# Performance work log

Hardware: AMD Instinct MI355X
Metric: run time of the kernel (lower is better)

The kernel has to match this reference:

```python
import jax, jax.numpy as jnp
import numpy as np


def gru_cell(x, h, Wi, Wh, bi, bh):
    # PyTorch GRU gate order: r, z, n
    gi = x @ Wi + bi
    gh = h @ Wh + bh
    ir, iz, inn = jnp.split(gi, 3, axis=-1)
    hr, hz, hn = jnp.split(gh, 3, axis=-1)
    r = jax.nn.sigmoid(ir + hr)
    z = jax.nn.sigmoid(iz + hz)
    n = jnp.tanh(inn + r * hn)
    return (1.0 - z) * n + z * h


def run_gru_dir(emb, lens, Wi, Wh, bi, bh, reverse):
    # Masked GRU emulating pack_padded_sequence: state holds once t >= len,
    # padded output positions are zero (as pad_packed_sequence produces).
    B, S, _ = emb.shape
    H = Wh.shape[0]
    xs = jnp.swapaxes(emb, 0, 1)  # [S, B, E]
    ts = jnp.arange(S)
    if reverse:
        xs = xs[::-1]
        ts = ts[::-1]
    def step(h, inp):
        x, t = inp
        valid = (t < lens)[:, None]
        h_new = jnp.where(valid, gru_cell(x, h, Wi, Wh, bi, bh), h)
        return h_new, jnp.where(valid, h_new, 0.0)
    hT, outs = jax.lax.scan(step, jnp.zeros((B, H), emb.dtype), (xs, ts))
    if reverse:
        outs = outs[::-1]
    return jnp.swapaxes(outs, 0, 1), hT  # [B,S,H], [B,H]


def seq2seq_forward(src, trg, src_lens, enc_embed, Wi_f, Wh_f, bi_f, bh_f,
                    Wi_b, Wh_b, bi_b, bh_b, W_e2d, b_e2d, dec_embed,
                    Wi_d, Wh_d, bi_d, bh_d, Wq, bq, Wk, bk, Wv, bv,
                    W1, b1, W2, b2):
    lens = jnp.clip(src_lens, 1, None)
    emb = enc_embed[src]  # [B,S,E]; dropout is identity in eval
    out_f, h_f = run_gru_dir(emb, lens, Wi_f, Wh_f, bi_f, bh_f, False)
    out_b, h_b = run_gru_dir(emb, lens, Wi_b, Wh_b, bi_b, bh_b, True)
    word_reps = jnp.concatenate([out_f, out_b], axis=-1)  # [B,S,2H]
    sent_rep = jnp.concatenate([h_f, h_b], axis=-1)       # [B,2H]
    hidden0 = jax.nn.gelu(sent_rep @ W_e2d + b_e2d, approximate=False)
    # k/v projections are loop-invariant -> hoist (same math as per-step)
    K = word_reps @ Wk + bk   # [B,S,kq]
    V = word_reps @ Wv + bv   # [B,S,D]
    scale = 1.0 / np.sqrt(Wq.shape[1]).astype(np.float32)
    def dec_step(h_prev, tok):
        e = dec_embed[tok]  # [B,E]
        h = gru_cell(e, h_prev, Wi_d, Wh_d, bi_d, bh_d)
        q = h @ Wq + bq
        alpha = jax.nn.softmax(jnp.einsum('bk,bsk->bs', q, K) * scale, axis=-1)
        attn = jnp.einsum('bs,bsd->bd', alpha, V)
        hid = h + attn
        out = jax.nn.gelu(hid @ W1 + b1, approximate=False) @ W2 + b2
        return hid, out
    toks = trg[:, :-1].T  # [T-1, B]
    _, outs = jax.lax.scan(dec_step, hidden0, toks)  # [T-1, B, V]
    B = trg.shape[0]
    V = W2.shape[1]
    # outputs[:, 0, :] stays zero as in the original preallocated buffer
    return jnp.concatenate(
        [jnp.zeros((B, 1, V), outs.dtype), jnp.swapaxes(outs, 0, 1)], axis=1)


def setup_inputs() -> dict:
    key = jax.random.key(0)
    ks = iter(jax.random.split(key, 32))
    B, S, T = 32, 64, 64
    SV, TV, E, H, D, KQ = 32000, 32000, 256, 512, 512, 64
    def nrm(shape, fan_in):
        return jax.random.normal(next(ks), shape, jnp.float32) / np.sqrt(fan_in).astype(np.float32)
    return {
        'src': jax.random.randint(next(ks), (B, S), 0, SV),
        'trg': jax.random.randint(next(ks), (B, T), 0, TV),
        'src_lens': jax.random.randint(next(ks), (B,), 1, S + 1),
        'enc_embed': jax.random.normal(next(ks), (SV, E), jnp.float32) * 0.1,
        'Wi_f': nrm((E, 3 * H), E), 'Wh_f': nrm((H, 3 * H), H),
        'bi_f': jnp.zeros((3 * H,), jnp.float32), 'bh_f': jnp.zeros((3 * H,), jnp.float32),
        'Wi_b': nrm((E, 3 * H), E), 'Wh_b': nrm((H, 3 * H), H),
        'bi_b': jnp.zeros((3 * H,), jnp.float32), 'bh_b': jnp.zeros((3 * H,), jnp.float32),
        'W_e2d': nrm((2 * H, D), 2 * H), 'b_e2d': jnp.zeros((D,), jnp.float32),
        'dec_embed': jax.random.normal(next(ks), (TV, E), jnp.float32) * 0.1,
        'Wi_d': nrm((E, 3 * D), E), 'Wh_d': nrm((D, 3 * D), D),
        'bi_d': jnp.zeros((3 * D,), jnp.float32), 'bh_d': jnp.zeros((3 * D,), jnp.float32),
        'Wq': nrm((D, KQ), D), 'bq': jnp.zeros((KQ,), jnp.float32),
        'Wk': nrm((2 * H, KQ), 2 * H), 'bk': jnp.zeros((KQ,), jnp.float32),
        'Wv': nrm((2 * H, D), 2 * H), 'bv': jnp.zeros((D,), jnp.float32),
        'W1': nrm((D, D), D), 'b1': jnp.zeros((D,), jnp.float32),
        'W2': nrm((D, TV), D), 'b2': jnp.zeros((TV,), jnp.float32),
    }


def reference(src, trg, src_lens, enc_embed, Wi_f, Wh_f, bi_f, bh_f,
              Wi_b, Wh_b, bi_b, bh_b, W_e2d, b_e2d, dec_embed,
              Wi_d, Wh_d, bi_d, bh_d, Wq, bq, Wk, bk, Wv, bv,
              W1, b1, W2, b2):
    return seq2seq_forward(src, trg, src_lens, enc_embed, Wi_f, Wh_f, bi_f, bh_f,
                           Wi_b, Wh_b, bi_b, bh_b, W_e2d, b_e2d, dec_embed,
                           Wi_d, Wh_d, bi_d, bh_d, Wq, bq, Wk, bk, Wv, bv,
                           W1, b1, W2, b2)
```

## Files before the change

### kernel.cpp

```cpp
#include <hip/hip_runtime.h>
#include <stdint.h>

typedef unsigned short u16;
typedef short v8s __attribute__((ext_vector_type(8)));
typedef float v4f __attribute__((ext_vector_type(4)));

#define DI static __device__ __forceinline__

DI u16 f2bf(float x){ union{float f; uint32_t u;} c; c.f = x; uint32_t r = c.u + 0x7fffu + ((c.u >> 16) & 1u); return (u16)(r >> 16); }
DI float bf2f(u16 b){ union{float f; uint32_t u;} c; c.u = ((uint32_t)b) << 16; return c.f; }
DI float gelu_f(float x){ return 0.5f * x * (1.0f + erff(x * 0.70710678118654752f)); }
DI float sigm(float x){ return 1.0f / (1.0f + expf(-x)); }

__global__ __launch_bounds__(256) void transpose_split_kernel(
    const float* __restrict__ W, u16* __restrict__ hi, u16* __restrict__ lo, int K, int N)
{
    __shared__ float t[32][33];
    int n0 = blockIdx.x * 32, k0 = blockIdx.y * 32;
    int tx = threadIdx.x & 31, ty = threadIdx.x >> 5;
    #pragma unroll
    for (int i = 0; i < 4; i++) {
        int k = k0 + ty + i * 8, n = n0 + tx;
        float v = (k < K && n < N) ? W[(size_t)k * N + n] : 0.f;
        t[ty + i * 8][tx] = v;
    }
    __syncthreads();
    #pragma unroll
    for (int i = 0; i < 4; i++) {
        int n = n0 + ty + i * 8, k = k0 + tx;
        if (n < N && k < K) {
            float v = t[tx][ty + i * 8];
            u16 h = f2bf(v);
            hi[(size_t)n * K + k] = h;
            lo[(size_t)n * K + k] = f2bf(v - bf2f(h));
        }
    }
}

__global__ __launch_bounds__(256) void gather_init_kernel(
    const int* __restrict__ src, const int* __restrict__ trg,
    const float* __restrict__ enc_embed, const float* __restrict__ dec_embed,
    float* __restrict__ embE, float* __restrict__ embD,
    float* __restrict__ hF0, float* __restrict__ hB0)
{
    int r = blockIdx.x, tx = threadIdx.x;
    if (r < 2048) {
        int idx = src[r];
        embE[(size_t)r * 256 + tx] = enc_embed[(size_t)idx * 256 + tx];
    } else if (r < 4064) {
        int rd = r - 2048;
        int t = rd >> 5, b = rd & 31;
        int tok = trg[b * 64 + t];
        embD[(size_t)rd * 256 + tx] = dec_embed[(size_t)tok * 256 + tx];
    } else {
        int i = (r - 4064) * 256 + tx;
        if (i < 16384) hF0[i] = 0.f; else hB0[i - 16384] = 0.f;
    }
}

__global__ __launch_bounds__(256) void gemm_bf16x3_kernel(
    const float* __restrict__ A, const u16* __restrict__ Bhi, const u16* __restrict__ Blo,
    const float* __restrict__ bias, float* __restrict__ C,
    int M, int N, int K, int act_gelu, int remap)
{
    __shared__ u16 Ah[128 * 40], Al[128 * 40], Bh[128 * 40], Bl[128 * 40];
    const int tid = threadIdx.x;
    const int lane = tid & 63, wave = tid >> 6;
    const int lm = lane & 15, quad = lane >> 4;
    const int wm = wave >> 1, wn = wave & 1;
    const int m0 = blockIdx.y * 128, n0 = blockIdx.x * 128;
    const int sr = tid >> 1;
    const int sh = (tid & 1) * 16;

    v4f acc[4][4];
    #pragma unroll
    for (int i = 0; i < 4; i++)
        #pragma unroll
        for (int j = 0; j < 4; j++)
            #pragma unroll
            for (int r = 0; r < 4; r++) acc[i][j][r] = 0.f;

    for (int k0 = 0; k0 < K; k0 += 32) {
        {
            float v[16];
            const int gm = m0 + sr;
            if (gm < M) {
                const float4* p = (const float4*)(A + (size_t)gm * K + k0 + sh);
                #pragma unroll
                for (int i = 0; i < 4; i++) {
                    float4 q = p[i];
                    v[4*i] = q.x; v[4*i+1] = q.y; v[4*i+2] = q.z; v[4*i+3] = q.w;
                }
            } else {
                #pragma unroll
                for (int i = 0; i < 16; i++) v[i] = 0.f;
            }
            v8s h0, h1, l0, l1;
            #pragma unroll
            for (int i = 0; i < 8; i++) {
                u16 ha = f2bf(v[i]);     u16 la = f2bf(v[i] - bf2f(ha));
                u16 hb = f2bf(v[8+i]);   u16 lb = f2bf(v[8+i] - bf2f(hb));
                h0[i] = (short)ha; l0[i] = (short)la; h1[i] = (short)hb; l1[i] = (short)lb;
            }
            *(v8s*)&Ah[sr * 40 + sh] = h0; *(v8s*)&Ah[sr * 40 + sh + 8] = h1;
            *(v8s*)&Al[sr * 40 + sh] = l0; *(v8s*)&Al[sr * 40 + sh + 8] = l1;
        }
        {
            const int gn = n0 + sr;
            v8s b0, b1, c0, c1;
            if (gn < N) {
                const v8s* ph = (const v8s*)(Bhi + (size_t)gn * K + k0 + sh);
                const v8s* pl = (const v8s*)(Blo + (size_t)gn * K + k0 + sh);
                b0 = ph[0]; b1 = ph[1]; c0 = pl[0]; c1 = pl[1];
            } else {
                #pragma unroll
                for (int i = 0; i < 8; i++) { b0[i] = 0; b1[i] = 0; c0[i] = 0; c1[i] = 0; }
            }
            *(v8s*)&Bh[sr * 40 + sh] = b0; *(v8s*)&Bh[sr * 40 + sh + 8] = b1;
            *(v8s*)&Bl[sr * 40 + sh] = c0; *(v8s*)&Bl[sr * 40 + sh + 8] = c1;
        }
        __syncthreads();
        v8s ah[4], al[4], bh[4], bl[4];
        #pragma unroll
        for (int mt = 0; mt < 4; mt++) {
            int off = (wm * 64 + mt * 16 + lm) * 40 + quad * 8;
            ah[mt] = *(v8s*)&Ah[off]; al[mt] = *(v8s*)&Al[off];
        }
        #pragma unroll
        for (int nt = 0; nt < 4; nt++) {
            int off = (wn * 64 + nt * 16 + lm) * 40 + quad * 8;
            bh[nt] = *(v8s*)&Bh[off]; bl[nt] = *(v8s*)&Bl[off];
        }
        #pragma unroll
        for (int mt = 0; mt < 4; mt++)
            #pragma unroll
            for (int nt = 0; nt < 4; nt++) {
                v4f a = acc[mt][nt];
                a = __builtin_amdgcn_mfma_f32_16x16x32_bf16(ah[mt], bh[nt], a, 0, 0, 0);
                a = __builtin_amdgcn_mfma_f32_16x16x32_bf16(ah[mt], bl[nt], a, 0, 0, 0);
                a = __builtin_amdgcn_mfma_f32_16x16x32_bf16(al[mt], bh[nt], a, 0, 0, 0);
                acc[mt][nt] = a;
            }
        __syncthreads();
    }
    #pragma unroll
    for (int nt = 0; nt < 4; nt++) {
        int col = n0 + wn * 64 + nt * 16 + lm;
        if (col >= N) continue;
        float bv = bias ? bias[col] : 0.f;
        #pragma unroll
        for (int mt = 0; mt < 4; mt++) {
            int rbase = m0 + wm * 64 + mt * 16 + quad * 4;
            #pragma unroll
            for (int r = 0; r < 4; r++) {
                int row = rbase + r;
                if (row < M) {
                    float v = acc[mt][nt][r] + bv;
                    if (act_gelu) v = gelu_f(v);
                    size_t drow = remap ? (size_t)((row & 31) * 64 + (row >> 5) + 1) : (size_t)row;
                    C[drow * (size_t)N + col] = v;
                }
            }
        }
    }
}

DI float gru_out(float i0, float i1, float i2, float g0, float g1, float g2,
                 float b0, float b1, float b2, float hprev)
{
    float r = sigm(i0 + g0 + b0);
    float z = sigm(i1 + g1 + b1);
    float n = tanhf(i2 + r * (g2 + b2));
    return (1.f - z) * n + z * hprev;
}

__global__ __launch_bounds__(256) void enc_step_kernel(
    int step,
    const float* __restrict__ hFin, float* __restrict__ hFout,
    const float* __restrict__ hBin, float* __restrict__ hBout,
    const float* __restrict__ giF, const float* __restrict__ giB,
    const float* __restrict__ Wh_f, const float* __restrict__ Wh_b,
    const float* __restrict__ bh_f, const float* __restrict__ bh_b,
    const int* __restrict__ src_lens,
    float* __restrict__ wrep, float* __restrict__ sent)
{
    const int dir = blockIdx.x >> 6;
    const int jb = (blockIdx.x & 63) * 8;
    const int tid = threadIdx.x;
    const int b = tid >> 3, jj = tid & 7, j = jb + jj;
    const float* hin = dir ? hBin : hFin;
    const float* gi  = dir ? giB : giF;
    const float* Wh  = dir ? Wh_b : Wh_f;
    const float* bh  = dir ? bh_b : bh_f;
    float* hout = dir ? hBout : hFout;
    const int t_eff = dir ? (63 - step) : step;

    __shared__ float hl[32 * 132];
    float g0 = 0.f, g1 = 0.f, g2 = 0.f;
    for (int kt = 0; kt < 512; kt += 128) {
        __syncthreads();
        #pragma unroll
        for (int w = 0; w < 4; w++) {
            int flat = (tid + w * 256) * 4;
            int bb = flat >> 7, kk = flat & 127;
            float4 fv = *(const float4*)(hin + bb * 512 + kt + kk);
            *(float4*)&hl[bb * 132 + kk] = fv;
        }
        __syncthreads();
        const float* w0base = Wh + (size_t)kt * 1536 + j;
        #pragma unroll 2
        for (int kk = 0; kk < 128; kk += 4) {
            float4 hv = *(const float4*)&hl[b * 132 + kk];
            const float* w = w0base + (size_t)kk * 1536;
            g0 += hv.x * w[0];    g1 += hv.x * w[512];  g2 += hv.x * w[1024];
            g0 += hv.y * w[1536]; g1 += hv.y * w[2048]; g2 += hv.y * w[2560];
            g0 += hv.z * w[3072]; g1 += hv.z * w[3584]; g2 += hv.z * w[4096];
            g0 += hv.w * w[4608]; g1 += hv.w * w[5120]; g2 += hv.w * w[5632];
        }
    }
    size_t gbase = ((size_t)b * 64 + t_eff) * 1536 + j;
    float hprev = hin[b * 512 + j];
    float hnew = gru_out(gi[gbase], gi[gbase + 512], gi[gbase + 1024],
                         g0, g1, g2, bh[j], bh[512 + j], bh[1024 + j], hprev);
    int len = src_lens[b]; if (len < 1) len = 1;
    bool valid = t_eff < len;
    float hkeep = valid ? hnew : hprev;
    hout[b * 512 + j] = hkeep;
    wrep[((size_t)b * 64 + t_eff) * 1024 + dir * 512 + j] = valid ? hnew : 0.f;
    if (step == 63) sent[b * 1024 + dir * 512 + j] = hkeep;
}

__global__ __launch_bounds__(256) void dec_cell_kernel(
    int t, const float* __restrict__ HID, const float* __restrict__ giD,
    const float* __restrict__ Wh, const float* __restrict__ bh,
    float* __restrict__ htmp)
{
    const int jb = blockIdx.x * 8;
    const int tid = threadIdx.x;
    const int b = tid >> 3, jj = tid & 7, j = jb + jj;
    const float* hin = HID + (size_t)t * 16384;

    __shared__ float hl[32 * 132];
    float g0 = 0.f, g1 = 0.f, g2 = 0.f;
    for (int kt = 0; kt < 512; kt += 128) {
        __syncthreads();
        #pragma unroll
        for (int w = 0; w < 4; w++) {
            int flat = (tid + w * 256) * 4;
            int bb = flat >> 7, kk = flat & 127;
            float4 fv = *(const float4*)(hin + bb * 512 + kt + kk);
            *(float4*)&hl[bb * 132 + kk] = fv;
        }
        __syncthreads();
        const float* w0base = Wh + (size_t)kt * 1536 + j;
        #pragma unroll 2
        for (int kk = 0; kk < 128; kk += 4) {
            float4 hv = *(const float4*)&hl[b * 132 + kk];
            const float* w = w0base + (size_t)kk * 1536;
            g0 += hv.x * w[0];    g1 += hv.x * w[512];  g2 += hv.x * w[1024];
            g0 += hv.y * w[1536]; g1 += hv.y * w[2048]; g2 += hv.y * w[2560];
            g0 += hv.z * w[3072]; g1 += hv.z * w[3584]; g2 += hv.z * w[4096];
            g0 += hv.w * w[4608]; g1 += hv.w * w[5120]; g2 += hv.w * w[5632];
        }
    }
    size_t gbase = ((size_t)t * 32 + b) * 1536 + j;
    float hprev = hin[b * 512 + j];
    float hnew = gru_out(giD[gbase], giD[gbase + 512], giD[gbase + 1024],
                         g0, g1, g2, bh[j], bh[512 + j], bh[1024 + j], hprev);
    htmp[b * 512 + j] = hnew;
}

__global__ __launch_bounds__(256) void dec_attn_kernel(
    int t, const float* __restrict__ htmp, const float* __restrict__ Kmat,
    const float* __restrict__ Vmat, const float* __restrict__ Wq,
    const float* __restrict__ bq, float* __restrict__ HID)
{
    const int b = blockIdx.x, tid = threadIdx.x;
    __shared__ float hl[512];
    __shared__ float Kt[64 * 68];
    __shared__ float qp[256];
    __shared__ float qv[64];
    __shared__ float aw[64];

    hl[tid] = htmp[b * 512 + tid];
    hl[256 + tid] = htmp[b * 512 + 256 + tid];
    #pragma unroll
    for (int w = 0; w < 4; w++) {
        int flat = (tid + w * 256) * 4;
        int s = flat >> 6, d = flat & 63;
        float4 fv = *(const float4*)(Kmat + ((size_t)b * 64 + s) * 64 + d);
        *(float4*)&Kt[s * 68 + d] = fv;
    }
    __syncthreads();
    {
        int o = tid >> 2, part = tid & 3;
        float acc = 0.f;
        const float* wq = Wq + (size_t)(part * 128) * 64 + o;
        int base = part * 128;
        for (int k = 0; k < 128; k++) acc += hl[base + k] * wq[(size_t)k * 64];
        qp[tid] = acc;
    }
    __syncthreads();
    if (tid < 64) qv[tid] = qp[tid * 4] + qp[tid * 4 + 1] + qp[tid * 4 + 2] + qp[tid * 4 + 3] + bq[tid];
    __syncthreads();
    if (tid < 64) {
        float sc = 0.f;
        #pragma unroll 8
        for (int d = 0; d < 64; d++) sc += qv[d] * Kt[tid * 68 + d];
        sc *= 0.125f;
        float mx = sc;
        #pragma unroll
        for (int m = 32; m >= 1; m >>= 1) mx = fmaxf(mx, __shfl_xor(mx, m));
        float e = expf(sc - mx);
        float sm = e;
        #pragma unroll
        for (int m = 32; m >= 1; m >>= 1) sm += __shfl_xor(sm, m);
        aw[tid] = e / sm;
    }
    __syncthreads();
    float* hid = HID + ((size_t)(t + 1)) * 16384 + (size_t)b * 512;
    #pragma unroll
    for (int c = 0; c < 2; c++) {
        int jcol = tid + c * 256;
        float acc = 0.f;
        for (int s = 0; s < 64; s++) acc += aw[s] * Vmat[((size_t)b * 64 + s) * 512 + jcol];
        hid[jcol] = hl[jcol] + acc;
    }
}

__global__ __launch_bounds__(256) void zero_col0_kernel(float* __restrict__ out)
{
    int gid = blockIdx.x * 256 + threadIdx.x;
    if (gid < 32 * 32000) {
        int b = gid / 32000, col = gid % 32000;
        out[(size_t)b * 64 * 32000 + col] = 0.f;
    }
}

extern "C" void kernel_launch(void* const* d_in, const int* in_sizes, int n_in,
                              void* d_out, int out_size, void* d_ws, size_t ws_size,
                              hipStream_t stream)
{
    const int*   src       = (const int*)d_in[0];
    const int*   trg       = (const int*)d_in[1];
    const int*   src_lens  = (const int*)d_in[2];
    const float* enc_embed = (const float*)d_in[3];
    const float* Wi_f  = (const float*)d_in[4];
    const float* Wh_f  = (const float*)d_in[5];
    const float* bi_f  = (const float*)d_in[6];
    const float* bh_f  = (const float*)d_in[7];
    const float* Wi_b  = (const float*)d_in[8];
    const float* Wh_b  = (const float*)d_in[9];
    const float* bi_b  = (const float*)d_in[10];
    const float* bh_b  = (const float*)d_in[11];
    const float* W_e2d = (const float*)d_in[12];
    const float* b_e2d = (const float*)d_in[13];
    const float* dec_embed = (const float*)d_in[14];
    const float* Wi_d  = (const float*)d_in[15];
    const float* Wh_d  = (const float*)d_in[16];
    const float* bi_d  = (const float*)d_in[17];
    const float* bh_d  = (const float*)d_in[18];
    const float* Wq    = (const float*)d_in[19];
    const float* bq    = (const float*)d_in[20];
    const float* Wk    = (const float*)d_in[21];
    const float* bk    = (const float*)d_in[22];
    const float* Wv    = (const float*)d_in[23];
    const float* bv    = (const float*)d_in[24];
    const float* W1    = (const float*)d_in[25];
    const float* b1    = (const float*)d_in[26];
    const float* W2    = (const float*)d_in[27];
    const float* b2    = (const float*)d_in[28];
    float* out = (float*)d_out;

    float* f = (float*)d_ws;
    float* embE = f; f += 524288;
    float* embD = f; f += 516096;
    float* giF  = f; f += 3145728;
    float* giB  = f; f += 3145728;
    float* giD  = f; f += 3096576;
    float* wrep = f; f += 2097152;
    float* sent = f; f += 32768;
    float* hF   = f; f += 32768;
    float* hB   = f; f += 32768;
    float* Kmat = f; f += 131072;
    float* Vmat = f; f += 1048576;
    float* HID  = f; f += 1048576;
    float* htmp = f; f += 16384;
    float* G1   = f; f += 1032192;
    u16* u = (u16*)f;
    u16* WiF_hi = u; u += 393216;  u16* WiF_lo = u; u += 393216;
    u16* WiB_hi = u; u += 393216;  u16* WiB_lo = u; u += 393216;
    u16* WiD_hi = u; u += 393216;  u16* WiD_lo = u; u += 393216;
    u16* Wk_hi  = u; u += 65536;   u16* Wk_lo  = u; u += 65536;
    u16* Wv_hi  = u; u += 524288;  u16* Wv_lo  = u; u += 524288;
    u16* We_hi  = u; u += 524288;  u16* We_lo  = u; u += 524288;
    u16* W1_hi  = u; u += 262144;  u16* W1_lo  = u; u += 262144;
    u16* W2_hi  = u; u += 16384000; u16* W2_lo = u; u += 16384000;

    hipLaunchKernelGGL(transpose_split_kernel, dim3(48, 8),   dim3(256), 0, stream, Wi_f,  WiF_hi, WiF_lo, 256, 1536);
    hipLaunchKernelGGL(transpose_split_kernel, dim3(48, 8),   dim3(256), 0, stream, Wi_b,  WiB_hi, WiB_lo, 256, 1536);
    hipLaunchKernelGGL(transpose_split_kernel, dim3(48, 8),   dim3(256), 0, stream, Wi_d,  WiD_hi, WiD_lo, 256, 1536);
    hipLaunchKernelGGL(transpose_split_kernel, dim3(2, 32),   dim3(256), 0, stream, Wk,    Wk_hi,  Wk_lo,  1024, 64);
    hipLaunchKernelGGL(transpose_split_kernel, dim3(16, 32),  dim3(256), 0, stream, Wv,    Wv_hi,  Wv_lo,  1024, 512);
    hipLaunchKernelGGL(transpose_split_kernel, dim3(16, 32),  dim3(256), 0, stream, W_e2d, We_hi,  We_lo,  1024, 512);
    hipLaunchKernelGGL(transpose_split_kernel, dim3(16, 16),  dim3(256), 0, stream, W1,    W1_hi,  W1_lo,  512, 512);
    hipLaunchKernelGGL(transpose_split_kernel, dim3(1000, 16),dim3(256), 0, stream, W2,    W2_hi,  W2_lo,  512, 32000);

    hipLaunchKernelGGL(gather_init_kernel, dim3(4192), dim3(256), 0, stream,
                       src, trg, enc_embed, dec_embed, embE, embD, hF, hB);

    hipLaunchKernelGGL(gemm_bf16x3_kernel, dim3(12, 16), dim3(256), 0, stream,
                       embE, WiF_hi, WiF_lo, bi_f, giF, 2048, 1536, 256, 0, 0);
    hipLaunchKernelGGL(gemm_bf16x3_kernel, dim3(12, 16), dim3(256), 0, stream,
                       embE, WiB_hi, WiB_lo, bi_b, giB, 2048, 1536, 256, 0, 0);
    hipLaunchKernelGGL(gemm_bf16x3_kernel, dim3(12, 16), dim3(256), 0, stream,
                       embD, WiD_hi, WiD_lo, bi_d, giD, 2016, 1536, 256, 0, 0);

    for (int step = 0; step < 64; step++) {
        const float* hFin = hF + (step & 1) * 16384;
        float*       hFout = hF + ((step + 1) & 1) * 16384;
        const float* hBin = hB + (step & 1) * 16384;
        float*       hBout = hB + ((step + 1) & 1) * 16384;
        hipLaunchKernelGGL(enc_step_kernel, dim3(128), dim3(256), 0, stream,
                           step, hFin, hFout, hBin, hBout, giF, giB,
                           Wh_f, Wh_b, bh_f, bh_b, src_lens, wrep, sent);
    }

    hipLaunchKernelGGL(gemm_bf16x3_kernel, dim3(1, 16), dim3(256), 0, stream,
                       wrep, Wk_hi, Wk_lo, bk, Kmat, 2048, 64, 1024, 0, 0);
    hipLaunchKernelGGL(gemm_bf16x3_kernel, dim3(4, 16), dim3(256), 0, stream,
                       wrep, Wv_hi, Wv_lo, bv, Vmat, 2048, 512, 1024, 0, 0);
    hipLaunchKernelGGL(gemm_bf16x3_kernel, dim3(4, 1), dim3(256), 0, stream,
                       sent, We_hi, We_lo, b_e2d, HID, 32, 512, 1024, 1, 0);

    for (int t = 0; t < 63; t++) {
        hipLaunchKernelGGL(dec_cell_kernel, dim3(64), dim3(256), 0, stream,
                           t, HID, giD, Wh_d, bh_d, htmp);
        hipLaunchKernelGGL(dec_attn_kernel, dim3(32), dim3(256), 0, stream,
                           t, htmp, Kmat, Vmat, Wq, bq, HID);
    }

    hipLaunchKernelGGL(gemm_bf16x3_kernel, dim3(4, 16), dim3(256), 0, stream,
                       HID + 16384, W1_hi, W1_lo, b1, G1, 2016, 512, 512, 1, 0);
    hipLaunchKernelGGL(gemm_bf16x3_kernel, dim3(250, 16), dim3(256), 0, stream,
                       G1, W2_hi, W2_lo, b2, out, 2016, 32000, 512, 0, 1);

    hipLaunchKernelGGL(zero_col0_kernel, dim3(4000), dim3(256), 0, stream, out);
}
```

Before: 4.244 ms.

## Make encoder and decoder recurrences persistent cooperative kernels with grid barriers

```diff
diff --git a/kernel.cpp b/kernel.cpp
--- a/kernel.cpp
+++ b/kernel.cpp
@@ -11,6 +11,15 @@
 DI float bf2f(u16 b){ union{float f; uint32_t u;} c; c.u = ((uint32_t)b) << 16; return c.f; }
 DI float gelu_f(float x){ return 0.5f * x * (1.0f + erff(x * 0.70710678118654752f)); }
 DI float sigm(float x){ return 1.0f / (1.0f + expf(-x)); }
+
+DI float gru_out(float i0, float i1, float i2, float g0, float g1, float g2,
+                 float b0, float b1, float b2, float hprev)
+{
+    float r = sigm(i0 + g0 + b0);
+    float z = sigm(i1 + g1 + b1);
+    float n = tanhf(i2 + r * (g2 + b2));
+    return (1.f - z) * n + z * hprev;
+}
 
 __global__ __launch_bounds__(256) void transpose_split_kernel(
     const float* __restrict__ W, u16* __restrict__ hi, u16* __restrict__ lo, int K, int N)
@@ -37,11 +46,31 @@
     }
 }
 
+__global__ __launch_bounds__(256) void transpose_f32_kernel(
+    const float* __restrict__ W, float* __restrict__ WT, int K, int N)
+{
+    __shared__ float t[32][33];
+    int n0 = blockIdx.x * 32, k0 = blockIdx.y * 32;
+    int tx = threadIdx.x & 31, ty = threadIdx.x >> 5;
+    #pragma unroll
+    for (int i = 0; i < 4; i++) {
+        int k = k0 + ty + i * 8, n = n0 + tx;
+        t[ty + i * 8][tx] = (k < K && n < N) ? W[(size_t)k * N + n] : 0.f;
+    }
+    __syncthreads();
+    #pragma unroll
+    for (int i = 0; i < 4; i++) {
+        int n = n0 + ty + i * 8, k = k0 + tx;
+        if (n < N && k < K) WT[(size_t)n * K + k] = t[tx][ty + i * 8];
+    }
+}
+
 __global__ __launch_bounds__(256) void gather_init_kernel(
     const int* __restrict__ src, const int* __restrict__ trg,
     const float* __restrict__ enc_embed, const float* __restrict__ dec_embed,
     float* __restrict__ embE, float* __restrict__ embD,
-    float* __restrict__ hF0, float* __restrict__ hB0)
+    float* __restrict__ hF0, float* __restrict__ hB0,
+    unsigned* __restrict__ bar)
 {
     int r = blockIdx.x, tx = threadIdx.x;
     if (r < 2048) {
@@ -52,23 +81,34 @@
         int t = rd >> 5, b = rd & 31;
         int tok = trg[b * 64 + t];
         embD[(size_t)rd * 256 + tx] = dec_embed[(size_t)tok * 256 + tx];
-    } else {
+    } else if (r < 4192) {
         int i = (r - 4064) * 256 + tx;
         if (i < 16384) hF0[i] = 0.f; else hB0[i - 16384] = 0.f;
+    } else {
+        if (tx < 16) bar[tx] = 0u;
     }
 }
 
 __global__ __launch_bounds__(256) void gemm_bf16x3_kernel(
     const float* __restrict__ A, const u16* __restrict__ Bhi, const u16* __restrict__ Blo,
     const float* __restrict__ bias, float* __restrict__ C,
-    int M, int N, int K, int act_gelu, int remap)
+    int M, int N, int K, int act_gelu, int remap, int swz)
 {
     __shared__ u16 Ah[128 * 40], Al[128 * 40], Bh[128 * 40], Bl[128 * 40];
     const int tid = threadIdx.x;
     const int lane = tid & 63, wave = tid >> 6;
     const int lm = lane & 15, quad = lane >> 4;
     const int wm = wave >> 1, wn = wave & 1;
-    const int m0 = blockIdx.y * 128, n0 = blockIdx.x * 128;
+    int tbx = blockIdx.x, tby = blockIdx.y;
+    if (swz) {
+        int nb = gridDim.x * gridDim.y;
+        int lin = tby * gridDim.x + tbx;
+        int per = nb >> 3;
+        int g = (lin & 7) * per + (lin >> 3);
+        tby = g % gridDim.y;
+        tbx = g / gridDim.y;
+    }
+    const int m0 = tby * 128, n0 = tbx * 128;
     const int sr = tid >> 1;
     const int sh = (tid & 1) * 16;
 
@@ -165,166 +205,189 @@
     }
 }
 
-DI float gru_out(float i0, float i1, float i2, float g0, float g1, float g2,
-                 float b0, float b1, float b2, float hprev)
-{
-    float r = sigm(i0 + g0 + b0);
-    float z = sigm(i1 + g1 + b1);
-    float n = tanhf(i2 + r * (g2 + b2));
-    return (1.f - z) * n + z * hprev;
-}
-
-__global__ __launch_bounds__(256) void enc_step_kernel(
-    int step,
-    const float* __restrict__ hFin, float* __restrict__ hFout,
-    const float* __restrict__ hBin, float* __restrict__ hBout,
+DI void grid_barrier(unsigned* ctr, unsigned target)
+{
+    __syncthreads();
+    if (threadIdx.x == 0) {
+        __hip_atomic_fetch_add(ctr, 1u, __ATOMIC_ACQ_REL, __HIP_MEMORY_SCOPE_AGENT);
+        while (__hip_atomic_load(ctr, __ATOMIC_RELAXED, __HIP_MEMORY_SCOPE_AGENT) < target)
+            __builtin_amdgcn_s_sleep(2);
+        __threadfence();
+    }
+    __syncthreads();
+}
+
+DI void stage_weights(const float* __restrict__ Wh, int jb, int tid, float* wl)
+{
+    for (int i = tid; i < 24 * 512; i += 256) {
+        int k = i / 24, c = i - k * 24;
+        wl[c * 512 + (k ^ ((c & 7) << 2))] =
+            Wh[(size_t)k * 1536 + (c >> 3) * 512 + jb + (c & 7)];
+    }
+}
+
+DI void gru_gates(const float* __restrict__ hin, float* hl,
+                  const float* w0, const float* w1, const float* w2,
+                  int tid, int b, int jj, float& g0, float& g1, float& g2)
+{
+    const int bsw = (b & 7) << 2;
+    const int jsw = jj << 2;
+    g0 = 0.f; g1 = 0.f; g2 = 0.f;
+    for (int kt = 0; kt < 512; kt += 128) {
+        __syncthreads();
+        #pragma unroll
+        for (int w = 0; w < 4; w++) {
+            int f4 = tid + w * 256;
+            int bb = f4 >> 5;
+            int kk = (f4 & 31) * 4;
+            float4 v = *(const float4*)(hin + bb * 512 + kt + kk);
+            *(float4*)&hl[bb * 128 + (kk ^ ((bb & 7) << 2))] = v;
+        }
+        __syncthreads();
+        const float* w0t = w0 + kt;
+        const float* w1t = w1 + kt;
+        const float* w2t = w2 + kt;
+        const float* hlb = &hl[b * 128];
+        #pragma unroll 4
+        for (int kk = 0; kk < 128; kk += 4) {
+            int ko = kk ^ jsw;
+            float4 hv = *(const float4*)&hlb[kk ^ bsw];
+            float4 a  = *(const float4*)(w0t + ko);
+            float4 c  = *(const float4*)(w1t + ko);
+            float4 d  = *(const float4*)(w2t + ko);
+            g0 += hv.x * a.x; g1 += hv.x * c.x; g2 += hv.x * d.x;
+            g0 += hv.y * a.y; g1 += hv.y * c.y; g2 += hv.y * d.y;
+            g0 += hv.z * a.z; g1 += hv.z * c.z; g2 += hv.z * d.z;
+            g0 += hv.w * a.w; g1 += hv.w * c.w; g2 += hv.w * d.w;
+        }
+    }
+}
+
+__global__ __launch_bounds__(256) void enc_persistent_kernel(
+    float* __restrict__ hF, float* __restrict__ hB,
     const float* __restrict__ giF, const float* __restrict__ giB,
     const float* __restrict__ Wh_f, const float* __restrict__ Wh_b,
     const float* __restrict__ bh_f, const float* __restrict__ bh_b,
     const int* __restrict__ src_lens,
-    float* __restrict__ wrep, float* __restrict__ sent)
-{
+    float* __restrict__ wrep, float* __restrict__ sent,
+    unsigned* __restrict__ bar)
+{
+    __shared__ float wl[24 * 512];
+    __shared__ float hl[32 * 128];
     const int dir = blockIdx.x >> 6;
     const int jb = (blockIdx.x & 63) * 8;
     const int tid = threadIdx.x;
     const int b = tid >> 3, jj = tid & 7, j = jb + jj;
-    const float* hin = dir ? hBin : hFin;
-    const float* gi  = dir ? giB : giF;
-    const float* Wh  = dir ? Wh_b : Wh_f;
-    const float* bh  = dir ? bh_b : bh_f;
-    float* hout = dir ? hBout : hFout;
-    const int t_eff = dir ? (63 - step) : step;
-
-    __shared__ float hl[32 * 132];
-    float g0 = 0.f, g1 = 0.f, g2 = 0.f;
-    for (int kt = 0; kt < 512; kt += 128) {
-        __syncthreads();
-        #pragma unroll
-        for (int w = 0; w < 4; w++) {
-            int flat = (tid + w * 256) * 4;
-            int bb = flat >> 7, kk = flat & 127;
-            float4 fv = *(const float4*)(hin + bb * 512 + kt + kk);
-            *(float4*)&hl[bb * 132 + kk] = fv;
-        }
-        __syncthreads();
-        const float* w0base = Wh + (size_t)kt * 1536 + j;
-        #pragma unroll 2
-        for (int kk = 0; kk < 128; kk += 4) {
-            float4 hv = *(const float4*)&hl[b * 132 + kk];
-            const float* w = w0base + (size_t)kk * 1536;
-            g0 += hv.x * w[0];    g1 += hv.x * w[512];  g2 += hv.x * w[1024];
-            g0 += hv.y * w[1536]; g1 += hv.y * w[2048]; g2 += hv.y * w[2560];
-            g0 += hv.z * w[3072]; g1 += hv.z * w[3584]; g2 += hv.z * w[4096];
-            g0 += hv.w * w[4608]; g1 += hv.w * w[5120]; g2 += hv.w * w[5632];
-        }
-    }
-    size_t gbase = ((size_t)b * 64 + t_eff) * 1536 + j;
-    float hprev = hin[b * 512 + j];
-    float hnew = gru_out(gi[gbase], gi[gbase + 512], gi[gbase + 1024],
-                         g0, g1, g2, bh[j], bh[512 + j], bh[1024 + j], hprev);
+    const float* gi = dir ? giB : giF;
+    const float* bh = dir ? bh_b : bh_f;
+    float* hbase = dir ? hB : hF;
+
+    stage_weights(dir ? Wh_b : Wh_f, jb, tid, wl);
     int len = src_lens[b]; if (len < 1) len = 1;
-    bool valid = t_eff < len;
-    float hkeep = valid ? hnew : hprev;
-    hout[b * 512 + j] = hkeep;
-    wrep[((size_t)b * 64 + t_eff) * 1024 + dir * 512 + j] = valid ? hnew : 0.f;
-    if (step == 63) sent[b * 1024 + dir * 512 + j] = hkeep;
-}
-
-__global__ __launch_bounds__(256) void dec_cell_kernel(
-    int t, const float* __restrict__ HID, const float* __restrict__ giD,
-    const float* __restrict__ Wh, const float* __restrict__ bh,
-    float* __restrict__ htmp)
-{
-    const int jb = blockIdx.x * 8;
-    const int tid = threadIdx.x;
-    const int b = tid >> 3, jj = tid & 7, j = jb + jj;
-    const float* hin = HID + (size_t)t * 16384;
-
-    __shared__ float hl[32 * 132];
-    float g0 = 0.f, g1 = 0.f, g2 = 0.f;
-    for (int kt = 0; kt < 512; kt += 128) {
-        __syncthreads();
-        #pragma unroll
-        for (int w = 0; w < 4; w++) {
-            int flat = (tid + w * 256) * 4;
-            int bb = flat >> 7, kk = flat & 127;
-            float4 fv = *(const float4*)(hin + bb * 512 + kt + kk);
-            *(float4*)&hl[bb * 132 + kk] = fv;
-        }
-        __syncthreads();
-        const float* w0base = Wh + (size_t)kt * 1536 + j;
-        #pragma unroll 2
-        for (int kk = 0; kk < 128; kk += 4) {
-            float4 hv = *(const float4*)&hl[b * 132 + kk];
-            const float* w = w0base + (size_t)kk * 1536;
-            g0 += hv.x * w[0];    g1 += hv.x * w[512];  g2 += hv.x * w[1024];
-            g0 += hv.y * w[1536]; g1 += hv.y * w[2048]; g2 += hv.y * w[2560];
-            g0 += hv.z * w[3072]; g1 += hv.z * w[3584]; g2 += hv.z * w[4096];
-            g0 += hv.w * w[4608]; g1 += hv.w * w[5120]; g2 += hv.w * w[5632];
-        }
-    }
-    size_t gbase = ((size_t)t * 32 + b) * 1536 + j;
-    float hprev = hin[b * 512 + j];
-    float hnew = gru_out(giD[gbase], giD[gbase + 512], giD[gbase + 1024],
-                         g0, g1, g2, bh[j], bh[512 + j], bh[1024 + j], hprev);
-    htmp[b * 512 + j] = hnew;
-}
-
-__global__ __launch_bounds__(256) void dec_attn_kernel(
-    int t, const float* __restrict__ htmp, const float* __restrict__ Kmat,
-    const float* __restrict__ Vmat, const float* __restrict__ Wq,
-    const float* __restrict__ bq, float* __restrict__ HID)
-{
-    const int b = blockIdx.x, tid = threadIdx.x;
-    __shared__ float hl[512];
-    __shared__ float Kt[64 * 68];
-    __shared__ float qp[256];
-    __shared__ float qv[64];
-    __shared__ float aw[64];
-
-    hl[tid] = htmp[b * 512 + tid];
-    hl[256 + tid] = htmp[b * 512 + 256 + tid];
-    #pragma unroll
-    for (int w = 0; w < 4; w++) {
-        int flat = (tid + w * 256) * 4;
-        int s = flat >> 6, d = flat & 63;
-        float4 fv = *(const float4*)(Kmat + ((size_t)b * 64 + s) * 64 + d);
-        *(float4*)&Kt[s * 68 + d] = fv;
-    }
-    __syncthreads();
-    {
-        int o = tid >> 2, part = tid & 3;
-        float acc = 0.f;
-        const float* wq = Wq + (size_t)(part * 128) * 64 + o;
-        int base = part * 128;
-        for (int k = 0; k < 128; k++) acc += hl[base + k] * wq[(size_t)k * 64];
-        qp[tid] = acc;
-    }
-    __syncthreads();
-    if (tid < 64) qv[tid] = qp[tid * 4] + qp[tid * 4 + 1] + qp[tid * 4 + 2] + qp[tid * 4 + 3] + bq[tid];
-    __syncthreads();
-    if (tid < 64) {
-        float sc = 0.f;
-        #pragma unroll 8
-        for (int d = 0; d < 64; d++) sc += qv[d] * Kt[tid * 68 + d];
-        sc *= 0.125f;
-        float mx = sc;
-        #pragma unroll
-        for (int m = 32; m >= 1; m >>= 1) mx = fmaxf(mx, __shfl_xor(mx, m));
-        float e = expf(sc - mx);
-        float sm = e;
-        #pragma unroll
-        for (int m = 32; m >= 1; m >>= 1) sm += __shfl_xor(sm, m);
-        aw[tid] = e / sm;
-    }
-    __syncthreads();
-    float* hid = HID + ((size_t)(t + 1)) * 16384 + (size_t)b * 512;
-    #pragma unroll
-    for (int c = 0; c < 2; c++) {
-        int jcol = tid + c * 256;
-        float acc = 0.f;
-        for (int s = 0; s < 64; s++) acc += aw[s] * Vmat[((size_t)b * 64 + s) * 512 + jcol];
-        hid[jcol] = hl[jcol] + acc;
+    const float bh0 = bh[j], bh1 = bh[512 + j], bh2 = bh[1024 + j];
+    const float* w0 = &wl[jj * 512];
+    const float* w1 = &wl[(8 + jj) * 512];
+    const float* w2 = &wl[(16 + jj) * 512];
+
+    for (int step = 0; step < 64; step++) {
+        const float* hin = hbase + (step & 1) * 16384;
+        float* hout = hbase + ((step + 1) & 1) * 16384;
+        const int t_eff = dir ? (63 - step) : step;
+        float g0, g1, g2;
+        gru_gates(hin, hl, w0, w1, w2, tid, b, jj, g0, g1, g2);
+        size_t gbase = ((size_t)b * 64 + t_eff) * 1536 + j;
+        float hprev = hin[b * 512 + j];
+        float hnew = gru_out(gi[gbase], gi[gbase + 512], gi[gbase + 1024],
+                             g0, g1, g2, bh0, bh1, bh2, hprev);
+        bool valid = t_eff < len;
+        float hkeep = valid ? hnew : hprev;
+        hout[b * 512 + j] = hkeep;
+        wrep[((size_t)b * 64 + t_eff) * 1024 + dir * 512 + j] = valid ? hnew : 0.f;
+        if (step == 63) sent[b * 1024 + dir * 512 + j] = hkeep;
+        else grid_barrier(bar, 128u * (unsigned)(step + 1));
+    }
+}
+
+__global__ __launch_bounds__(256) void dec_persistent_kernel(
+    float* __restrict__ HID, const float* __restrict__ giD,
+    const float* __restrict__ Wh_d, const float* __restrict__ bh_d,
+    const float* __restrict__ Kmat, const float* __restrict__ Vmat,
+    const float* __restrict__ WqT, const float* __restrict__ bq,
+    float* __restrict__ htmp, unsigned* __restrict__ bar)
+{
+    __shared__ float wl[24 * 512];
+    __shared__ float pool[32 * 128];
+    const int bx = blockIdx.x, tid = threadIdx.x;
+    const int b = tid >> 3, jj = tid & 7, j = bx * 8 + jj;
+    const int bb = bx >> 1, half = bx & 1;
+    float* hb = pool;
+    float* qp = pool + 512;
+    float* qv = pool + 768;
+    float* aw = pool + 832;
+
+    stage_weights(Wh_d, bx * 8, tid, wl);
+    const float bh0 = bh_d[j], bh1 = bh_d[512 + j], bh2 = bh_d[1024 + j];
+    const float* w0 = &wl[jj * 512];
+    const float* w1 = &wl[(8 + jj) * 512];
+    const float* w2 = &wl[(16 + jj) * 512];
+
+    for (int t = 0; t < 63; t++) {
+        const float* hin = HID + (size_t)t * 16384;
+        float g0, g1, g2;
+        gru_gates(hin, pool, w0, w1, w2, tid, b, jj, g0, g1, g2);
+        size_t gbase = ((size_t)t * 32 + b) * 1536 + j;
+        float hprev = hin[b * 512 + j];
+        float hnew = gru_out(giD[gbase], giD[gbase + 512], giD[gbase + 1024],
+                             g0, g1, g2, bh0, bh1, bh2, hprev);
+        htmp[b * 512 + j] = hnew;
+        grid_barrier(bar, 64u * (unsigned)(2 * t + 1));
+
+        hb[tid] = htmp[bb * 512 + tid];
+        hb[256 + tid] = htmp[bb * 512 + 256 + tid];
+        __syncthreads();
+        {
+            int o = tid >> 2, part = tid & 3;
+            const float* wq = WqT + (size_t)o * 512 + part * 128;
+            const float* hh = hb + part * 128;
+            float acc = 0.f;
+            #pragma unroll 4
+            for (int k = 0; k < 128; k += 4) {
+                float4 w = *(const float4*)(wq + k);
+                acc += hh[k]*w.x + hh[k+1]*w.y + hh[k+2]*w.z + hh[k+3]*w.w;
+            }
+            qp[tid] = acc;
+        }
+        __syncthreads();
+        if (tid < 64) qv[tid] = qp[tid*4] + qp[tid*4+1] + qp[tid*4+2] + qp[tid*4+3] + bq[tid];
+        __syncthreads();
+        if (tid < 64) {
+            const float* kr = Kmat + ((size_t)bb * 64 + tid) * 64;
+            float sc = 0.f;
+            #pragma unroll
+            for (int d = 0; d < 64; d += 4) {
+                float4 kv = *(const float4*)(kr + d);
+                sc += qv[d]*kv.x + qv[d+1]*kv.y + qv[d+2]*kv.z + qv[d+3]*kv.w;
+            }
+            sc *= 0.125f;
+            float mx = sc;
+            #pragma unroll
+            for (int m = 32; m >= 1; m >>= 1) mx = fmaxf(mx, __shfl_xor(mx, m));
+            float e = expf(sc - mx);
+            float sm = e;
+            #pragma unroll
+            for (int m = 32; m >= 1; m >>= 1) sm += __shfl_xor(sm, m);
+            aw[tid] = e / sm;
+        }
+        __syncthreads();
+        {
+            int jcol = half * 256 + tid;
+            const float* vp = Vmat + (size_t)bb * 32768 + jcol;
+            float acc = 0.f;
+            #pragma unroll 8
+            for (int s = 0; s < 64; s++) acc += aw[s] * vp[(size_t)s * 512];
+            HID[(size_t)(t + 1) * 16384 + (size_t)bb * 512 + jcol] = hb[jcol] + acc;
+        }
+        if (t < 62) grid_barrier(bar, 64u * (unsigned)(2 * t + 2));
     }
 }
 
@@ -387,6 +450,8 @@
     float* HID  = f; f += 1048576;
     float* htmp = f; f += 16384;
     float* G1   = f; f += 1032192;
+    float* WqT  = f; f += 32768;
+    unsigned* bar = (unsigned*)f; f += 16;
     u16* u = (u16*)f;
     u16* WiF_hi = u; u += 393216;  u16* WiF_lo = u; u += 393216;
     u16* WiB_hi = u; u += 393216;  u16* WiB_lo = u; u += 393216;
@@ -405,45 +470,46 @@
     hipLaunchKernelGGL(transpose_split_kernel, dim3(16, 32),  dim3(256), 0, stream, W_e2d, We_hi,  We_lo,  1024, 512);
     hipLaunchKernelGGL(transpose_split_kernel, dim3(16, 16),  dim3(256), 0, stream, W1,    W1_hi,  W1_lo,  512, 512);
     hipLaunchKernelGGL(transpose_split_kernel, dim3(1000, 16),dim3(256), 0, stream, W2,    W2_hi,  W2_lo,  512, 32000);
-
-    hipLaunchKernelGGL(gather_init_kernel, dim3(4192), dim3(256), 0, stream,
-                       src, trg, enc_embed, dec_embed, embE, embD, hF, hB);
+    hipLaunchKernelGGL(transpose_f32_kernel,   dim3(2, 16),   dim3(256), 0, stream, Wq,    WqT,    512, 64);
+
+    hipLaunchKernelGGL(gather_init_kernel, dim3(4193), dim3(256), 0, stream,
+                       src, trg, enc_embed, dec_embed, embE, embD, hF, hB, bar);
 
     hipLaunchKernelGGL(gemm_bf16x3_kernel, dim3(12, 16), dim3(256), 0, stream,
-                       embE, WiF_hi, WiF_lo, bi_f, giF, 2048, 1536, 256, 0, 0);
+                       embE, WiF_hi, WiF_lo, bi_f, giF, 2048, 1536, 256, 0, 0, 1);
     hipLaunchKernelGGL(gemm_bf16x3_kernel, dim3(12, 16), dim3(256), 0, stream,
-                       embE, WiB_hi, WiB_lo, bi_b, giB, 2048, 1536, 256, 0, 0);
+                       embE, WiB_hi, WiB_lo, bi_b, giB, 2048, 1536, 256, 0, 0, 1);
     hipLaunchKernelGGL(gemm_bf16x3_kernel, dim3(12, 16), dim3(256), 0, stream,
-                       embD, WiD_hi, WiD_lo, bi_d, giD, 2016, 1536, 256, 0, 0);
-
-    for (int step = 0; step < 64; step++) {
-        const float* hFin = hF + (step & 1) * 16384;
-        float*       hFout = hF + ((step + 1) & 1) * 16384;
-        const float* hBin = hB + (step & 1) * 16384;
-        float*       hBout = hB + ((step + 1) & 1) * 16384;
-        hipLaunchKernelGGL(enc_step_kernel, dim3(128), dim3(256), 0, stream,
-                           step, hFin, hFout, hBin, hBout, giF, giB,
-                           Wh_f, Wh_b, bh_f, bh_b, src_lens, wrep, sent);
+                       embD, WiD_hi, WiD_lo, bi_d, giD, 2016, 1536, 256, 0, 0, 1);
+
+    {
+        void* eargs[] = { (void*)&hF, (void*)&hB, (void*)&giF, (void*)&giB,
+                          (void*)&Wh_f, (void*)&Wh_b, (void*)&bh_f, (void*)&bh_b,
+                          (void*)&src_lens, (void*)&wrep, (void*)&sent, (void*)&bar };
+        hipLaunchCooperativeKernel((const void*)enc_persistent_kernel,
+                                   dim3(128), dim3(256), eargs, 0, stream);
     }
 
     hipLaunchKernelGGL(gemm_bf16x3_kernel, dim3(1, 16), dim3(256), 0, stream,
-                       wrep, Wk_hi, Wk_lo, bk, Kmat, 2048, 64, 1024, 0, 0);
+                       wrep, Wk_hi, Wk_lo, bk, Kmat, 2048, 64, 1024, 0, 0, 0);
     hipLaunchKernelGGL(gemm_bf16x3_kernel, dim3(4, 16), dim3(256), 0, stream,
-                       wrep, Wv_hi, Wv_lo, bv, Vmat, 2048, 512, 1024, 0, 0);
+                       wrep, Wv_hi, Wv_lo, bv, Vmat, 2048, 512, 1024, 0, 0, 1);
     hipLaunchKernelGGL(gemm_bf16x3_kernel, dim3(4, 1), dim3(256), 0, stream,
-                       sent, We_hi, We_lo, b_e2d, HID, 32, 512, 1024, 1, 0);
-
-    for (int t = 0; t < 63; t++) {
-        hipLaunchKernelGGL(dec_cell_kernel, dim3(64), dim3(256), 0, stream,
-                           t, HID, giD, Wh_d, bh_d, htmp);
-        hipLaunchKernelGGL(dec_attn_kernel, dim3(32), dim3(256), 0, stream,
-                           t, htmp, Kmat, Vmat, Wq, bq, HID);
+                       sent, We_hi, We_lo, b_e2d, HID, 32, 512, 1024, 1, 0, 0);
+
+    {
+        unsigned* barD = bar + 1;
+        void* dargs[] = { (void*)&HID, (void*)&giD, (void*)&Wh_d, (void*)&bh_d,
+                          (void*)&Kmat, (void*)&Vmat, (void*)&WqT, (void*)&bq,
+                          (void*)&htmp, (void*)&barD };
+        hipLaunchCooperativeKernel((const void*)dec_persistent_kernel,
+                                   dim3(64), dim3(256), dargs, 0, stream);
     }
 
     hipLaunchKernelGGL(gemm_bf16x3_kernel, dim3(4, 16), dim3(256), 0, stream,
-                       HID + 16384, W1_hi, W1_lo, b1, G1, 2016, 512, 512, 1, 0);
+                       HID + 16384, W1_hi, W1_lo, b1, G1, 2016, 512, 512, 1, 0, 1);
     hipLaunchKernelGGL(gemm_bf16x3_kernel, dim3(250, 16), dim3(256), 0, stream,
-                       G1, W2_hi, W2_lo, b2, out, 2016, 32000, 512, 0, 1);
+                       G1, W2_hi, W2_lo, b2, out, 2016, 32000, 512, 0, 1, 1);
 
     hipLaunchKernelGGL(zero_col0_kernel, dim3(4000), dim3(256), 0, stream, out);
 }
```

Measured after the change: 4.083 ms. -3.8%, faster.
